# Optimization experiments

Measured on AMD Instinct MI355X. Metric: run time of the kernel, lower is better.

Reference implementation:

```python
import jax, jax.numpy as jnp
import numpy as np

C = 64            # x_channel (d_model)
D = 2 * C         # d_inner (expand=2)
N = C // 2        # d_state
K = 4             # scan directions
R = -(-C // 16)   # dt_rank = ceil(d_model/16)
Bsz, H, W = 2, 48, 48
EPS = 1e-5


def setup_inputs() -> dict:
    key = jax.random.key(0)
    ks = jax.random.split(key, 8)
    g = lambda k, shp, s: jax.random.normal(k, shp, dtype=jnp.float32) * s
    return {
        "fufea1": g(ks[0], (Bsz, C, H, W), 1.0),
        "ln_g": jnp.ones((C,), jnp.float32),
        "ln_b": jnp.zeros((C,), jnp.float32),
        "in_proj_w": g(ks[1], (2 * D, C), C ** -0.5),
        "conv_w": g(ks[2], (D, 1, 3, 3), 1.0 / 3.0),   # depthwise 3x3
        "conv_b": g(ks[3], (D,), 0.02),
        "x_proj_w": g(ks[4], (K, R + 2 * N, D), D ** -0.5),
        "dt_w": g(ks[5], (K, D, R), R ** -0.5),
        "dt_b": g(ks[6], (K, D), 0.1),
        "A_logs": jnp.log(jnp.tile(jnp.arange(1, N + 1, dtype=jnp.float32), (K, D, 1))),  # S4D-real init
        "Ds": jnp.ones((K, D), jnp.float32),
        "out_ln_g": jnp.ones((D,), jnp.float32),
        "out_ln_b": jnp.zeros((D,), jnp.float32),
        "out_proj_w": g(ks[7], (C, D), D ** -0.5),
    }


def _layernorm(x, g, b):
    mu = x.mean(-1, keepdims=True)
    var = ((x - mu) ** 2).mean(-1, keepdims=True)
    return (x - mu) * jax.lax.rsqrt(var + EPS) * g + b


def reference(fufea1, ln_g, ln_b, in_proj_w, conv_w, conv_b, x_proj_w,
              dt_w, dt_b, A_logs, Ds, out_ln_g, out_ln_b, out_proj_w):
    B, Cc, Hh, Ww = fufea1.shape
    L = Hh * Ww
    # pre-LN (over channels, channels-last)
    xn = _layernorm(fufea1.transpose(0, 2, 3, 1), ln_g, ln_b)          # (B,H,W,C)
    # SS2D: in_proj -> split x,z
    xz = xn @ in_proj_w.T                                               # (B,H,W,2D)
    x, z = jnp.split(xz, 2, axis=-1)
    x = x.transpose(0, 3, 1, 2)                                         # (B,D,H,W)
    x = jax.lax.conv_general_dilated(x, conv_w, (1, 1), "SAME",
                                     feature_group_count=D,
                                     dimension_numbers=("NCHW", "OIHW", "NCHW"))
    x = jax.nn.silu(x + conv_b[None, :, None, None])
    # 4-direction sequences: row-major, col-major, and their reverses
    x_hw = x.reshape(B, D, L)
    x_wh = x.transpose(0, 1, 3, 2).reshape(B, D, L)
    xs = jnp.stack([x_hw, x_wh], axis=1)                                # (B,2,D,L)
    xs = jnp.concatenate([xs, jnp.flip(xs, axis=-1)], axis=1)           # (B,K,D,L)
    # per-direction projections of dt, B, C
    x_dbl = jnp.einsum("bkdl,kcd->bkcl", xs, x_proj_w)
    dts, Bs, Cs = jnp.split(x_dbl, [R, R + N], axis=2)                  # (B,K,R,L),(B,K,N,L),(B,K,N,L)
    dts = jnp.einsum("bkrl,kdr->bkdl", dts, dt_w)
    delta = jax.nn.softplus(dts + dt_b[None, :, :, None])               # (B,K,D,L)
    A = -jnp.exp(A_logs)                                                # (K,D,N)
    # selective scan over L; carry h: (B,K,D,N)
    u_l = xs.transpose(3, 0, 1, 2)                                      # (L,B,K,D)
    dt_l = delta.transpose(3, 0, 1, 2)
    B_l = Bs.transpose(3, 0, 1, 2)                                      # (L,B,K,N)
    C_l = Cs.transpose(3, 0, 1, 2)

    def step(h, inp):
        u_t, d_t, b_t, c_t = inp
        dA = jnp.exp(d_t[..., None] * A)                                # (B,K,D,N)
        h = dA * h + (d_t * u_t)[..., None] * b_t[:, :, None, :]
        y = jnp.einsum("bkdn,bkn->bkd", h, c_t)
        return h, y

    h0 = jnp.zeros((B, K, D, N), xs.dtype)
    _, ys = jax.lax.scan(step, h0, (u_l, dt_l, B_l, C_l))               # ys: (L,B,K,D)
    out_y = ys.transpose(1, 2, 3, 0) + Ds[None, :, :, None] * xs        # (B,K,D,L)
    # merge the 4 directions back to row-major hw order
    inv_y = jnp.flip(out_y[:, 2:4], axis=-1)                            # (B,2,D,L)
    wh = lambda t: t.reshape(B, D, Ww, Hh).transpose(0, 1, 3, 2).reshape(B, D, L)
    y = out_y[:, 0] + inv_y[:, 0] + wh(out_y[:, 1]) + wh(inv_y[:, 1])   # (B,D,L)
    y = y.transpose(0, 2, 1).reshape(B, Hh, Ww, D)
    y = _layernorm(y, out_ln_g, out_ln_b) * jax.nn.silu(z)
    out = (y @ out_proj_w.T).transpose(0, 3, 1, 2) + fufea1             # residual add
    return out
```

## Files before the change

### kernel.cpp

```cpp
#include <hip/hip_runtime.h>

#define Cc 64
#define Dd 128
#define Nn 32
#define Kk 4
#define Rr 4
#define Bb 2
#define Hh 48
#define Ww 48
#define Ll 2304
#define EPSf 1e-5f
#define LCc 144

#if __has_builtin(__builtin_amdgcn_exp2f)
#define EXP2F __builtin_amdgcn_exp2f
#else
#define EXP2F exp2f
#endif

__device__ __forceinline__ float wsum64(float v) {
  v += __shfl_xor(v, 32);
  v += __shfl_xor(v, 16);
  v += __shfl_xor(v, 8);
  v += __shfl_xor(v, 4);
  v += __shfl_xor(v, 2);
  v += __shfl_xor(v, 1);
  return v;
}

__device__ __forceinline__ float hmax32(float v) {
  v = fmaxf(v, __shfl_xor(v, 1));
  v = fmaxf(v, __shfl_xor(v, 2));
  v = fmaxf(v, __shfl_xor(v, 4));
  v = fmaxf(v, __shfl_xor(v, 8));
  v = fmaxf(v, __shfl_xor(v, 16));
  return v;
}

__global__ __launch_bounds__(256) void k1_ln_inproj(
    const float* __restrict__ x, const float* __restrict__ g,
    const float* __restrict__ bta, const float* __restrict__ Wp,
    float* __restrict__ xin, float* __restrict__ zb)
{
  __shared__ float xS[16][65];
  __shared__ float xnS[16][64];
  __shared__ float xaS[128][17];
  const int tid = threadIdx.x;
  const int wv = tid >> 6, lane = tid & 63;
  const int pbase = blockIdx.x * 16;
  const int b = pbase / Ll;
  const int lbase = pbase % Ll;
  {
    const int c = tid >> 2, li0 = (tid & 3) * 4;
    const float4 v4 = *(const float4*)&x[(b * Cc + c) * Ll + lbase + li0];
    xS[li0 + 0][c] = v4.x;
    xS[li0 + 1][c] = v4.y;
    xS[li0 + 2][c] = v4.z;
    xS[li0 + 3][c] = v4.w;
  }
  __syncthreads();
  const float gv = g[lane], bv = bta[lane];
  for (int pi = 0; pi < 4; ++pi) {
    const int p = wv * 4 + pi;
    const float v = xS[p][lane];
    const float mu = wsum64(v) * (1.0f / 64.0f);
    const float dv = v - mu;
    const float var = wsum64(dv * dv) * (1.0f / 64.0f);
    const float rs = rsqrtf(var + EPSf);
    xnS[p][lane] = dv * rs * gv + bv;
  }
  __syncthreads();
  float acc[4][4];
  #pragma unroll
  for (int pi = 0; pi < 4; ++pi)
    #pragma unroll
    for (int m = 0; m < 4; ++m) acc[pi][m] = 0.f;
  const float4* W4 = (const float4*)Wp;
  #pragma unroll 4
  for (int c4 = 0; c4 < 16; ++c4) {
    float4 xn4[4];
    #pragma unroll
    for (int pi = 0; pi < 4; ++pi)
      xn4[pi] = ((const float4*)xnS[wv * 4 + pi])[c4];
    #pragma unroll
    for (int m = 0; m < 4; ++m) {
      const float4 w4 = W4[(lane + 64 * m) * 16 + c4];
      #pragma unroll
      for (int pi = 0; pi < 4; ++pi)
        acc[pi][m] += xn4[pi].x * w4.x + xn4[pi].y * w4.y +
                      xn4[pi].z * w4.z + xn4[pi].w * w4.w;
    }
  }
  #pragma unroll
  for (int pi = 0; pi < 4; ++pi) {
    const int l = lbase + wv * 4 + pi;
    zb[(b * Ll + l) * Dd + lane]      = acc[pi][2];
    zb[(b * Ll + l) * Dd + lane + 64] = acc[pi][3];
    xaS[lane][wv * 4 + pi]      = acc[pi][0];
    xaS[lane + 64][wv * 4 + pi] = acc[pi][1];
  }
  __syncthreads();
  const int d = tid >> 1, off = (tid & 1) * 8;
  float* dst = &xin[(b * Dd + d) * Ll + lbase + off];
  #pragma unroll
  for (int i = 0; i < 8; ++i) dst[i] = xaS[d][off + i];
}

__global__ __launch_bounds__(512) void k3_proj(
    const float* __restrict__ xin, const float* __restrict__ cw,
    const float* __restrict__ cb, const float* __restrict__ xpw,
    const float* __restrict__ dtw, const float* __restrict__ dtb,
    float* __restrict__ xc, float2* __restrict__ dd2,
    float* __restrict__ Bm, float* __restrict__ Cm)
{
  __shared__ float xinS[128][30];
  __shared__ float xvS[8][132];
  __shared__ float dtsS[8][16];
  const int t = threadIdx.x;
  const int pb = blockIdx.x * 8;
  const int b = pb / Ll;
  const int lb = pb % Ll;
  const int h0 = lb / Ww, w0 = lb % Ww;
  for (int i = t; i < 3840; i += 512) {
    const int d = i / 30, j = i % 30;
    const int r = j / 10, c = j % 10;
    const int hh = h0 + r - 1, ww = w0 + c - 1;
    float v = 0.f;
    if (hh >= 0 && hh < Hh && ww >= 0 && ww < Ww)
      v = xin[(b * Dd + d) * Ll + hh * Ww + ww];
    xinS[d][j] = v;
  }
  __syncthreads();
  for (int i = t; i < 1024; i += 512) {
    const int pi = i >> 7, d = i & 127;
    float acc = cb[d];
    #pragma unroll
    for (int r = 0; r < 3; ++r)
      #pragma unroll
      for (int c = 0; c < 3; ++c)
        acc += xinS[d][r * 10 + pi + c] * cw[d * 9 + r * 3 + c];
    const float sig = 1.0f / (1.0f + __expf(-acc));
    xvS[pi][d] = acc * sig;
  }
  __syncthreads();
  for (int i = t; i < 1024; i += 512) {
    const int d = i >> 3, pi = i & 7;
    xc[(b * Dd + d) * Ll + lb + pi] = xvS[pi][d];
  }
  if (t < 272) {
    const int k = t / 68, c = t % 68;
    const size_t bkL = (size_t)(b * Kk + k) * Ll;
    float acc[8];
    #pragma unroll
    for (int pi = 0; pi < 8; ++pi) acc[pi] = 0.f;
    const float4* w4p = (const float4*)(xpw + (k * 68 + c) * 128);
    for (int d4 = 0; d4 < 32; ++d4) {
      const float4 w4 = w4p[d4];
      #pragma unroll
      for (int pi = 0; pi < 8; ++pi) {
        const float4 x4 = ((const float4*)xvS[pi])[d4];
        acc[pi] += x4.x * w4.x + x4.y * w4.y + x4.z * w4.z + x4.w * w4.w;
      }
    }
    #pragma unroll
    for (int pi = 0; pi < 8; ++pi) {
      const int l0 = lb + pi;
      const int h = l0 / Ww, w = l0 % Ww;
      int lk;
      if      (k == 0) lk = l0;
      else if (k == 1) lk = w * Hh + h;
      else if (k == 2) lk = Ll - 1 - l0;
      else             lk = Ll - 1 - (w * Hh + h);
      if (c < Rr)            dtsS[pi][k * 4 + c] = acc[pi];
      else if (c < Rr + Nn)  Bm[(bkL + lk) * Nn + (c - Rr)] = acc[pi];
      else                   Cm[(bkL + lk) * Nn + (c - Rr - Nn)] = acc[pi];
    }
  }
  __syncthreads();
  {
    const int k = t >> 7, dd = t & 127;
    const float4 dw = *(const float4*)&dtw[(k * Dd + dd) * 4];
    const float biasv = dtb[k * Dd + dd];
    float2* drow = dd2 + ((size_t)((b * Kk + k) * Dd) + dd) * Ll;
    float2 buf[8];
    #pragma unroll
    for (int pi = 0; pi < 8; ++pi) {
      const float a = biasv
          + dtsS[pi][k * 4 + 0] * dw.x + dtsS[pi][k * 4 + 1] * dw.y
          + dtsS[pi][k * 4 + 2] * dw.z + dtsS[pi][k * 4 + 3] * dw.w;
      const float sp = (a > 20.f) ? a : log1pf(__expf(a));
      buf[pi] = make_float2(sp, sp * xvS[pi][dd]);
    }
    if (k == 0) {
      float4* f4 = (float4*)(drow + lb);
      #pragma unroll
      for (int j = 0; j < 4; ++j)
        f4[j] = make_float4(buf[2 * j].x, buf[2 * j].y, buf[2 * j + 1].x, buf[2 * j + 1].y);
    } else if (k == 2) {
      float4* f4 = (float4*)(drow + (Ll - 8 - lb));
      #pragma unroll
      for (int j = 0; j < 4; ++j)
        f4[j] = make_float4(buf[7 - 2 * j].x, buf[7 - 2 * j].y, buf[6 - 2 * j].x, buf[6 - 2 * j].y);
    } else {
      #pragma unroll
      for (int pi = 0; pi < 8; ++pi) {
        const int l0 = lb + pi;
        const int h = l0 / Ww, w = l0 % Ww;
        int lk = w * Hh + h;
        if (k == 3) lk = Ll - 1 - lk;
        drow[lk] = buf[pi];
      }
    }
  }
}

__global__ __launch_bounds__(512) void k4_scan(
    const float2* __restrict__ dd2, const float* __restrict__ Bm,
    const float* __restrict__ Cm, const float* __restrict__ Alogs,
    float* __restrict__ ys)
{
  __shared__ float hendS[16][32];
  __shared__ float carryS[16][32];
  __shared__ float sumDS[16];
  __shared__ float cmaxS[16];
  __shared__ float pS[16][8][36];
  const int tid = threadIdx.x;
  const int s = tid >> 5, n = tid & 31;
  const int blk = blockIdx.x;
  const int bk = blk & 7;
  const int d = blk >> 3;
  const int b = bk >> 2, k = bk & 3;
  const float An = -__expf(Alogs[(k * Dd + d) * Nn + n]);
  const float AnE = An * 1.44269504f;
  const size_t bkL = (size_t)(b * Kk + k) * Ll;
  const float2* dP = dd2 + ((size_t)((b * Kk + k) * Dd) + d) * Ll;
  const float* bP = Bm + bkL * Nn + n;
  const float* cP = Cm + bkL * Nn + n;
  const int lbeg = s * LCc;
  float* yP = ys + ((size_t)((b * Kk + k) * Dd) + d) * Ll + lbeg;
  const int rrow = n & 7, qtr = n >> 3;

  float h = 0.f, sumD = 0.f, cmx = 0.f;
  {
    const float4* q4 = (const float4*)(dP + lbeg);
    const float* bl = bP + (size_t)lbeg * Nn;
    const float* cl = cP + (size_t)lbeg * Nn;
    float4 qa = q4[0], qb = q4[1];
    float b0 = bl[0], b1 = bl[Nn], b2 = bl[2 * Nn], b3 = bl[3 * Nn];
    float c0 = cl[0], c1 = cl[Nn], c2 = cl[2 * Nn], c3 = cl[3 * Nn];
    for (int t8 = 0; t8 < LCc / 8; ++t8) {
      #pragma unroll
      for (int half = 0; half < 2; ++half) {
        q4 += 2; bl += 4 * Nn; cl += 4 * Nn;
        const float4 qa_n = q4[0], qb_n = q4[1];
        const float b0n = bl[0], b1n = bl[Nn], b2n = bl[2 * Nn], b3n = bl[3 * Nn];
        const float c0n = cl[0], c1n = cl[Nn], c2n = cl[2 * Nn], c3n = cl[3 * Nn];
        h = EXP2F(qa.x * AnE) * h + qa.y * b0; pS[s][half * 4 + 0][n] = h * c0;
        h = EXP2F(qa.z * AnE) * h + qa.w * b1; pS[s][half * 4 + 1][n] = h * c1;
        h = EXP2F(qb.x * AnE) * h + qb.y * b2; pS[s][half * 4 + 2][n] = h * c2;
        h = EXP2F(qb.z * AnE) * h + qb.w * b3; pS[s][half * 4 + 3][n] = h * c3;
        sumD += (qa.x + qa.z) + (qb.x + qb.z);
        cmx = fmaxf(cmx, fmaxf(fmaxf(fabsf(c0), fabsf(c1)),
                               fmaxf(fabsf(c2), fabsf(c3))));
        qa = qa_n; qb = qb_n; b0 = b0n; b1 = b1n; b2 = b2n; b3 = b3n;
        c0 = c0n; c1 = c1n; c2 = c2n; c3 = c3n;
      }
      const float4 a4 = *(const float4*)&pS[s][rrow][qtr * 8];
      const float4 d4v = *(const float4*)&pS[s][rrow][qtr * 8 + 4];
      float sum = ((a4.x + a4.y) + (a4.z + a4.w)) + ((d4v.x + d4v.y) + (d4v.z + d4v.w));
      sum += __shfl_xor(sum, 8);
      sum += __shfl_xor(sum, 16);
      if (n < 8) yP[t8 * 8 + n] = sum;
    }
  }
  hendS[s][n] = h;
  const float cmxAll = hmax32(cmx);
  if (n == 0) { sumDS[s] = sumD; cmaxS[s] = cmxAll; }
  __syncthreads();
  if (tid < 32) {
    float carry = 0.f;
    #pragma unroll
    for (int s2 = 0; s2 < 16; ++s2) {
      carryS[s2][tid] = carry;
      carry = EXP2F(AnE * sumDS[s2]) * carry + hendS[s2][tid];
    }
  }
  __syncthreads();
  const float carry = carryS[s][n];
  const float mc = hmax32(fabsf(carry));
  const float AmaxE = hmax32(AnE);
  const float Pstop = log2f(mc * cmaxS[s] * 3.2e6f) / (-AmaxE);
  {
    float hc = carry, P = 0.f;
    const float4* q4 = (const float4*)(dP + lbeg);
    const float* cl = cP + (size_t)lbeg * Nn;
    for (int t8 = 0; t8 < LCc / 8; ++t8) {
      if (!(P < Pstop)) break;
      #pragma unroll
      for (int half = 0; half < 2; ++half) {
        const float4 qa = q4[0], qb = q4[1];
        q4 += 2;
        hc *= EXP2F(qa.x * AnE); pS[s][half * 4 + 0][n] = hc * cl[0];
        hc *= EXP2F(qa.z * AnE); pS[s][half * 4 + 1][n] = hc * cl[Nn];
        hc *= EXP2F(qb.x * AnE); pS[s][half * 4 + 2][n] = hc * cl[2 * Nn];
        hc *= EXP2F(qb.z * AnE); pS[s][half * 4 + 3][n] = hc * cl[3 * Nn];
        P += (qa.x + qa.z) + (qb.x + qb.z);
        cl += 4 * Nn;
      }
      const float4 a4 = *(const float4*)&pS[s][rrow][qtr * 8];
      const float4 d4v = *(const float4*)&pS[s][rrow][qtr * 8 + 4];
      float sum = ((a4.x + a4.y) + (a4.z + a4.w)) + ((d4v.x + d4v.y) + (d4v.z + d4v.w));
      sum += __shfl_xor(sum, 8);
      sum += __shfl_xor(sum, 16);
      if (n < 8) yP[t8 * 8 + n] += sum;
    }
  }
}

__global__ __launch_bounds__(256) void k5_merge(
    const float* __restrict__ ys, const float* __restrict__ zb,
    const float* __restrict__ og, const float* __restrict__ ob,
    const float* __restrict__ Wo, const float* __restrict__ resid,
    const float* __restrict__ xc, const float* __restrict__ DsP,
    float* __restrict__ out)
{
  __shared__ float ysS[4][16][128];
  __shared__ float tS[16][128];
  __shared__ float oS[64][17];
  __shared__ float xcS[16][128];
  const int tid = threadIdx.x;
  const int wv = tid >> 6, lane = tid & 63;
  const int pbase = blockIdx.x * 16;
  const int b = pbase / Ll;
  const int lbase = pbase % Ll;
  const int hrow = lbase / Ww, w0 = lbase % Ww;
  {
    const int dch = tid & 127, seg = tid >> 7;
    {
      const float4 a4 = *(const float4*)&xc[(b * Dd + dch) * Ll + lbase + seg * 8];
      const float4 c4 = *(const float4*)&xc[(b * Dd + dch) * Ll + lbase + seg * 8 + 4];
      xcS[seg * 8 + 0][dch] = a4.x; xcS[seg * 8 + 1][dch] = a4.y;
      xcS[seg * 8 + 2][dch] = a4.z; xcS[seg * 8 + 3][dch] = a4.w;
      xcS[seg * 8 + 4][dch] = c4.x; xcS[seg * 8 + 5][dch] = c4.y;
      xcS[seg * 8 + 6][dch] = c4.z; xcS[seg * 8 + 7][dch] = c4.w;
    }
    {
      const size_t r0 = ((size_t)(b * Kk + 0) * Dd + dch) * Ll + lbase + seg * 8;
      const float4 a4 = *(const float4*)&ys[r0];
      const float4 c4 = *(const float4*)&ys[r0 + 4];
      ysS[0][seg * 8 + 0][dch] = a4.x; ysS[0][seg * 8 + 1][dch] = a4.y;
      ysS[0][seg * 8 + 2][dch] = a4.z; ysS[0][seg * 8 + 3][dch] = a4.w;
      ysS[0][seg * 8 + 4][dch] = c4.x; ysS[0][seg * 8 + 5][dch] = c4.y;
      ysS[0][seg * 8 + 6][dch] = c4.z; ysS[0][seg * 8 + 7][dch] = c4.w;
    }
    {
      const size_t r2 = ((size_t)(b * Kk + 2) * Dd + dch) * Ll + (Ll - 16 - lbase) + seg * 8;
      const float4 a4 = *(const float4*)&ys[r2];
      const float4 c4 = *(const float4*)&ys[r2 + 4];
      ysS[2][15 - seg * 8 - 0][dch] = a4.x; ysS[2][15 - seg * 8 - 1][dch] = a4.y;
      ysS[2][15 - seg * 8 - 2][dch] = a4.z; ysS[2][15 - seg * 8 - 3][dch] = a4.w;
      ysS[2][15 - seg * 8 - 4][dch] = c4.x; ysS[2][15 - seg * 8 - 5][dch] = c4.y;
      ysS[2][15 - seg * 8 - 6][dch] = c4.z; ysS[2][15 - seg * 8 - 7][dch] = c4.w;
    }
    {
      const size_t r1 = ((size_t)(b * Kk + 1) * Dd + dch) * Ll;
      const size_t r3 = ((size_t)(b * Kk + 3) * Dd + dch) * Ll;
      #pragma unroll
      for (int j = 0; j < 8; ++j) {
        const int p = seg * 8 + j;
        const int l1 = (w0 + p) * Hh + hrow;
        ysS[1][p][dch] = ys[r1 + l1];
        ysS[3][p][dch] = ys[r3 + (Ll - 1 - l1)];
      }
    }
  }
  float sDs[2];
  #pragma unroll
  for (int m = 0; m < 2; ++m) {
    const int dch = lane + 64 * m;
    sDs[m] = DsP[dch] + DsP[Dd + dch] + DsP[2 * Dd + dch] + DsP[3 * Dd + dch];
  }
  __syncthreads();
  for (int pi = 0; pi < 4; ++pi) {
    const int p = wv * 4 + pi;
    const int l0 = lbase + p;
    float tv[2];
    #pragma unroll
    for (int m = 0; m < 2; ++m) {
      const int dch = lane + 64 * m;
      tv[m] = ysS[0][p][dch] + ysS[1][p][dch] + ysS[2][p][dch] + ysS[3][p][dch]
            + sDs[m] * xcS[p][dch];
    }
    const float mu = wsum64(tv[0] + tv[1]) * (1.0f / 128.0f);
    const float q = wsum64((tv[0] - mu) * (tv[0] - mu) +
                           (tv[1] - mu) * (tv[1] - mu)) * (1.0f / 128.0f);
    const float rs = rsqrtf(q + EPSf);
    #pragma unroll
    for (int m = 0; m < 2; ++m) {
      const int dch = lane + 64 * m;
      const float zz = zb[(size_t)(b * Ll + l0) * Dd + dch];
      const float sig = 1.0f / (1.0f + __expf(-zz));
      tS[p][dch] = ((tv[m] - mu) * rs * og[dch] + ob[dch]) * (zz * sig);
    }
  }
  __syncthreads();
  float acc[4] = {0.f, 0.f, 0.f, 0.f};
  const float4* W4 = (const float4*)Wo;
  for (int d4 = 0; d4 < 32; ++d4) {
    const float4 w4 = W4[lane * 32 + d4];
    #pragma unroll
    for (int pi = 0; pi < 4; ++pi) {
      const float4 t4 = ((const float4*)tS[wv * 4 + pi])[d4];
      acc[pi] += t4.x * w4.x + t4.y * w4.y + t4.z * w4.z + t4.w * w4.w;
    }
  }
  #pragma unroll
  for (int pi = 0; pi < 4; ++pi) oS[lane][wv * 4 + pi] = acc[pi];
  __syncthreads();
  const int c = tid >> 2, off = (tid & 3) * 4;
  const size_t obase = (size_t)(b * Cc + c) * Ll + lbase + off;
  const float4 r4 = *(const float4*)(resid + obase);
  float4 o4;
  o4.x = oS[c][off + 0] + r4.x;
  o4.y = oS[c][off + 1] + r4.y;
  o4.z = oS[c][off + 2] + r4.z;
  o4.w = oS[c][off + 3] + r4.w;
  *(float4*)(out + obase) = o4;
}

extern "C" void kernel_launch(void* const* d_in, const int* in_sizes, int n_in,
                              void* d_out, int out_size, void* d_ws, size_t ws_size,
                              hipStream_t stream)
{
  (void)in_sizes; (void)n_in; (void)out_size; (void)ws_size;
  const float* fufea1     = (const float*)d_in[0];
  const float* ln_g       = (const float*)d_in[1];
  const float* ln_b       = (const float*)d_in[2];
  const float* in_proj_w  = (const float*)d_in[3];
  const float* conv_w     = (const float*)d_in[4];
  const float* conv_b     = (const float*)d_in[5];
  const float* x_proj_w   = (const float*)d_in[6];
  const float* dt_w       = (const float*)d_in[7];
  const float* dt_b       = (const float*)d_in[8];
  const float* A_logs     = (const float*)d_in[9];
  const float* Ds         = (const float*)d_in[10];
  const float* out_ln_g   = (const float*)d_in[11];
  const float* out_ln_b   = (const float*)d_in[12];
  const float* out_proj_w = (const float*)d_in[13];

  float* ws = (float*)d_ws;
  float2* dd2 = (float2*)ws;
  float* Bm   = ws + 4718592;
  float* Cm   = ws + 5308416;
  float* zb   = ws + 5898240;
  float* xc   = ws + 6488064;
  float* ysb  = ws + 7077888;
  float* xin  = ws + 7077888;

  k1_ln_inproj<<<288, 256, 0, stream>>>(fufea1, ln_g, ln_b, in_proj_w, xin, zb);
  k3_proj<<<576, 512, 0, stream>>>(xin, conv_w, conv_b, x_proj_w, dt_w, dt_b,
                                   xc, dd2, Bm, Cm);
  k4_scan<<<1024, 512, 0, stream>>>(dd2, Bm, Cm, A_logs, ysb);
  k5_merge<<<288, 256, 0, stream>>>(ysb, zb, out_ln_g, out_ln_b, out_proj_w, fufea1,
                                    xc, Ds, (float*)d_out);
}
```

Baseline: 202.6 us.

## Interleave B and C projections, tile merge kernel as 4x4 patches, overlap xc stores

B and C are stored interleaved as float2 pairs, so the scan loads one 8-byte value per step instead of two separate 4-byte loads from different arrays. The merge kernel now handles 4x4 spatial tiles instead of 16-pixel row segments, so the column-major directions can be read with float4 loads instead of strided scalar gathers. In the projection kernel, threads that sit idle during the x_proj GEMV now write xc in parallel with it. This costs more index arithmetic and a strided write pattern for the interleaved buffer.

```diff
diff --git a/kernel.cpp b/kernel.cpp
--- a/kernel.cpp
+++ b/kernel.cpp
@@ -111,7 +111,7 @@
     const float* __restrict__ cb, const float* __restrict__ xpw,
     const float* __restrict__ dtw, const float* __restrict__ dtb,
     float* __restrict__ xc, float2* __restrict__ dd2,
-    float* __restrict__ Bm, float* __restrict__ Cm)
+    float* __restrict__ BCm)
 {
   __shared__ float xinS[128][30];
   __shared__ float xvS[8][132];
@@ -143,10 +143,6 @@
     xvS[pi][d] = acc * sig;
   }
   __syncthreads();
-  for (int i = t; i < 1024; i += 512) {
-    const int d = i >> 3, pi = i & 7;
-    xc[(b * Dd + d) * Ll + lb + pi] = xvS[pi][d];
-  }
   if (t < 272) {
     const int k = t / 68, c = t % 68;
     const size_t bkL = (size_t)(b * Kk + k) * Ll;
@@ -171,9 +167,17 @@
       else if (k == 1) lk = w * Hh + h;
       else if (k == 2) lk = Ll - 1 - l0;
       else             lk = Ll - 1 - (w * Hh + h);
-      if (c < Rr)            dtsS[pi][k * 4 + c] = acc[pi];
-      else if (c < Rr + Nn)  Bm[(bkL + lk) * Nn + (c - Rr)] = acc[pi];
-      else                   Cm[(bkL + lk) * Nn + (c - Rr - Nn)] = acc[pi];
+      if (c < Rr)
+        dtsS[pi][k * 4 + c] = acc[pi];
+      else if (c < Rr + Nn)
+        BCm[((bkL + lk) * Nn + (c - Rr)) * 2]     = acc[pi];
+      else
+        BCm[((bkL + lk) * Nn + (c - Rr - Nn)) * 2 + 1] = acc[pi];
+    }
+  } else {
+    for (int i = t - 272; i < 1024; i += 240) {
+      const int d = i >> 3, pi = i & 7;
+      xc[(b * Dd + d) * Ll + lb + pi] = xvS[pi][d];
     }
   }
   __syncthreads();
@@ -215,9 +219,8 @@
 }
 
 __global__ __launch_bounds__(512) void k4_scan(
-    const float2* __restrict__ dd2, const float* __restrict__ Bm,
-    const float* __restrict__ Cm, const float* __restrict__ Alogs,
-    float* __restrict__ ys)
+    const float2* __restrict__ dd2, const float* __restrict__ BCm,
+    const float* __restrict__ Alogs, float* __restrict__ ys)
 {
   __shared__ float hendS[16][32];
   __shared__ float carryS[16][32];
@@ -234,8 +237,7 @@
   const float AnE = An * 1.44269504f;
   const size_t bkL = (size_t)(b * Kk + k) * Ll;
   const float2* dP = dd2 + ((size_t)((b * Kk + k) * Dd) + d) * Ll;
-  const float* bP = Bm + bkL * Nn + n;
-  const float* cP = Cm + bkL * Nn + n;
+  const float2* bcP = (const float2*)BCm + bkL * Nn + n;
   const int lbeg = s * LCc;
   float* yP = ys + ((size_t)((b * Kk + k) * Dd) + d) * Ll + lbeg;
   const int rrow = n & 7, qtr = n >> 3;
@@ -243,27 +245,23 @@
   float h = 0.f, sumD = 0.f, cmx = 0.f;
   {
     const float4* q4 = (const float4*)(dP + lbeg);
-    const float* bl = bP + (size_t)lbeg * Nn;
-    const float* cl = cP + (size_t)lbeg * Nn;
+    const float2* bcl = bcP + (size_t)lbeg * Nn;
     float4 qa = q4[0], qb = q4[1];
-    float b0 = bl[0], b1 = bl[Nn], b2 = bl[2 * Nn], b3 = bl[3 * Nn];
-    float c0 = cl[0], c1 = cl[Nn], c2 = cl[2 * Nn], c3 = cl[3 * Nn];
+    float2 bc0 = bcl[0], bc1 = bcl[Nn], bc2 = bcl[2 * Nn], bc3 = bcl[3 * Nn];
     for (int t8 = 0; t8 < LCc / 8; ++t8) {
       #pragma unroll
       for (int half = 0; half < 2; ++half) {
-        q4 += 2; bl += 4 * Nn; cl += 4 * Nn;
+        q4 += 2; bcl += 4 * Nn;
         const float4 qa_n = q4[0], qb_n = q4[1];
-        const float b0n = bl[0], b1n = bl[Nn], b2n = bl[2 * Nn], b3n = bl[3 * Nn];
-        const float c0n = cl[0], c1n = cl[Nn], c2n = cl[2 * Nn], c3n = cl[3 * Nn];
-        h = EXP2F(qa.x * AnE) * h + qa.y * b0; pS[s][half * 4 + 0][n] = h * c0;
-        h = EXP2F(qa.z * AnE) * h + qa.w * b1; pS[s][half * 4 + 1][n] = h * c1;
-        h = EXP2F(qb.x * AnE) * h + qb.y * b2; pS[s][half * 4 + 2][n] = h * c2;
-        h = EXP2F(qb.z * AnE) * h + qb.w * b3; pS[s][half * 4 + 3][n] = h * c3;
+        const float2 bc0n = bcl[0], bc1n = bcl[Nn], bc2n = bcl[2 * Nn], bc3n = bcl[3 * Nn];
+        h = EXP2F(qa.x * AnE) * h + qa.y * bc0.x; pS[s][half * 4 + 0][n] = h * bc0.y;
+        h = EXP2F(qa.z * AnE) * h + qa.w * bc1.x; pS[s][half * 4 + 1][n] = h * bc1.y;
+        h = EXP2F(qb.x * AnE) * h + qb.y * bc2.x; pS[s][half * 4 + 2][n] = h * bc2.y;
+        h = EXP2F(qb.z * AnE) * h + qb.w * bc3.x; pS[s][half * 4 + 3][n] = h * bc3.y;
         sumD += (qa.x + qa.z) + (qb.x + qb.z);
-        cmx = fmaxf(cmx, fmaxf(fmaxf(fabsf(c0), fabsf(c1)),
-                               fmaxf(fabsf(c2), fabsf(c3))));
-        qa = qa_n; qb = qb_n; b0 = b0n; b1 = b1n; b2 = b2n; b3 = b3n;
-        c0 = c0n; c1 = c1n; c2 = c2n; c3 = c3n;
+        cmx = fmaxf(cmx, fmaxf(fmaxf(fabsf(bc0.y), fabsf(bc1.y)),
+                               fmaxf(fabsf(bc2.y), fabsf(bc3.y))));
+        qa = qa_n; qb = qb_n; bc0 = bc0n; bc1 = bc1n; bc2 = bc2n; bc3 = bc3n;
       }
       const float4 a4 = *(const float4*)&pS[s][rrow][qtr * 8];
       const float4 d4v = *(const float4*)&pS[s][rrow][qtr * 8 + 4];
@@ -293,17 +291,17 @@
   {
     float hc = carry, P = 0.f;
     const float4* q4 = (const float4*)(dP + lbeg);
-    const float* cl = cP + (size_t)lbeg * Nn;
+    const float2* cl = bcP + (size_t)lbeg * Nn;
     for (int t8 = 0; t8 < LCc / 8; ++t8) {
       if (!(P < Pstop)) break;
       #pragma unroll
       for (int half = 0; half < 2; ++half) {
         const float4 qa = q4[0], qb = q4[1];
         q4 += 2;
-        hc *= EXP2F(qa.x * AnE); pS[s][half * 4 + 0][n] = hc * cl[0];
-        hc *= EXP2F(qa.z * AnE); pS[s][half * 4 + 1][n] = hc * cl[Nn];
-        hc *= EXP2F(qb.x * AnE); pS[s][half * 4 + 2][n] = hc * cl[2 * Nn];
-        hc *= EXP2F(qb.z * AnE); pS[s][half * 4 + 3][n] = hc * cl[3 * Nn];
+        hc *= EXP2F(qa.x * AnE); pS[s][half * 4 + 0][n] = hc * cl[0].y;
+        hc *= EXP2F(qa.z * AnE); pS[s][half * 4 + 1][n] = hc * cl[Nn].y;
+        hc *= EXP2F(qb.x * AnE); pS[s][half * 4 + 2][n] = hc * cl[2 * Nn].y;
+        hc *= EXP2F(qb.z * AnE); pS[s][half * 4 + 3][n] = hc * cl[3 * Nn].y;
         P += (qa.x + qa.z) + (qb.x + qb.z);
         cl += 4 * Nn;
       }
@@ -330,48 +328,40 @@
   __shared__ float xcS[16][128];
   const int tid = threadIdx.x;
   const int wv = tid >> 6, lane = tid & 63;
-  const int pbase = blockIdx.x * 16;
-  const int b = pbase / Ll;
-  const int lbase = pbase % Ll;
-  const int hrow = lbase / Ww, w0 = lbase % Ww;
+  const int tb = blockIdx.x;
+  const int b = tb / 144;
+  const int ti = tb % 144;
+  const int tr = ti / 12, tc = ti % 12;
+  const int h0 = tr * 4, w0 = tc * 4;
   {
-    const int dch = tid & 127, seg = tid >> 7;
-    {
-      const float4 a4 = *(const float4*)&xc[(b * Dd + dch) * Ll + lbase + seg * 8];
-      const float4 c4 = *(const float4*)&xc[(b * Dd + dch) * Ll + lbase + seg * 8 + 4];
-      xcS[seg * 8 + 0][dch] = a4.x; xcS[seg * 8 + 1][dch] = a4.y;
-      xcS[seg * 8 + 2][dch] = a4.z; xcS[seg * 8 + 3][dch] = a4.w;
-      xcS[seg * 8 + 4][dch] = c4.x; xcS[seg * 8 + 5][dch] = c4.y;
-      xcS[seg * 8 + 6][dch] = c4.z; xcS[seg * 8 + 7][dch] = c4.w;
-    }
-    {
-      const size_t r0 = ((size_t)(b * Kk + 0) * Dd + dch) * Ll + lbase + seg * 8;
-      const float4 a4 = *(const float4*)&ys[r0];
-      const float4 c4 = *(const float4*)&ys[r0 + 4];
-      ysS[0][seg * 8 + 0][dch] = a4.x; ysS[0][seg * 8 + 1][dch] = a4.y;
-      ysS[0][seg * 8 + 2][dch] = a4.z; ysS[0][seg * 8 + 3][dch] = a4.w;
-      ysS[0][seg * 8 + 4][dch] = c4.x; ysS[0][seg * 8 + 5][dch] = c4.y;
-      ysS[0][seg * 8 + 6][dch] = c4.z; ysS[0][seg * 8 + 7][dch] = c4.w;
-    }
-    {
-      const size_t r2 = ((size_t)(b * Kk + 2) * Dd + dch) * Ll + (Ll - 16 - lbase) + seg * 8;
-      const float4 a4 = *(const float4*)&ys[r2];
-      const float4 c4 = *(const float4*)&ys[r2 + 4];
-      ysS[2][15 - seg * 8 - 0][dch] = a4.x; ysS[2][15 - seg * 8 - 1][dch] = a4.y;
-      ysS[2][15 - seg * 8 - 2][dch] = a4.z; ysS[2][15 - seg * 8 - 3][dch] = a4.w;
-      ysS[2][15 - seg * 8 - 4][dch] = c4.x; ysS[2][15 - seg * 8 - 5][dch] = c4.y;
-      ysS[2][15 - seg * 8 - 6][dch] = c4.z; ysS[2][15 - seg * 8 - 7][dch] = c4.w;
-    }
-    {
-      const size_t r1 = ((size_t)(b * Kk + 1) * Dd + dch) * Ll;
-      const size_t r3 = ((size_t)(b * Kk + 3) * Dd + dch) * Ll;
-      #pragma unroll
-      for (int j = 0; j < 8; ++j) {
-        const int p = seg * 8 + j;
-        const int l1 = (w0 + p) * Hh + hrow;
-        ysS[1][p][dch] = ys[r1 + l1];
-        ysS[3][p][dch] = ys[r3 + (Ll - 1 - l1)];
-      }
+    const int dch = tid & 127, half = tid >> 7;
+    #pragma unroll
+    for (int ii = 0; ii < 2; ++ii) {
+      const int i = half * 2 + ii;
+      const int l0 = (h0 + i) * Ww + w0;
+      float4 v;
+      v = *(const float4*)&xc[(b * Dd + dch) * Ll + l0];
+      xcS[i * 4 + 0][dch] = v.x; xcS[i * 4 + 1][dch] = v.y;
+      xcS[i * 4 + 2][dch] = v.z; xcS[i * 4 + 3][dch] = v.w;
+      v = *(const float4*)&ys[((size_t)(b * Kk + 0) * Dd + dch) * Ll + l0];
+      ysS[0][i * 4 + 0][dch] = v.x; ysS[0][i * 4 + 1][dch] = v.y;
+      ysS[0][i * 4 + 2][dch] = v.z; ysS[0][i * 4 + 3][dch] = v.w;
+      const int r2 = Ll - 4 - (h0 + i) * Ww - w0;
+      v = *(const float4*)&ys[((size_t)(b * Kk + 2) * Dd + dch) * Ll + r2];
+      ysS[2][i * 4 + 3][dch] = v.x; ysS[2][i * 4 + 2][dch] = v.y;
+      ysS[2][i * 4 + 1][dch] = v.z; ysS[2][i * 4 + 0][dch] = v.w;
+    }
+    #pragma unroll
+    for (int jj = 0; jj < 2; ++jj) {
+      const int j = half * 2 + jj;
+      const int l1 = (w0 + j) * Hh + h0;
+      float4 v = *(const float4*)&ys[((size_t)(b * Kk + 1) * Dd + dch) * Ll + l1];
+      ysS[1][0 * 4 + j][dch] = v.x; ysS[1][1 * 4 + j][dch] = v.y;
+      ysS[1][2 * 4 + j][dch] = v.z; ysS[1][3 * 4 + j][dch] = v.w;
+      const int r3 = Ll - 4 - (w0 + j) * Hh - h0;
+      v = *(const float4*)&ys[((size_t)(b * Kk + 3) * Dd + dch) * Ll + r3];
+      ysS[3][3 * 4 + j][dch] = v.x; ysS[3][2 * 4 + j][dch] = v.y;
+      ysS[3][1 * 4 + j][dch] = v.z; ysS[3][0 * 4 + j][dch] = v.w;
     }
   }
   float sDs[2];
@@ -383,7 +373,7 @@
   __syncthreads();
   for (int pi = 0; pi < 4; ++pi) {
     const int p = wv * 4 + pi;
-    const int l0 = lbase + p;
+    const int l0 = (h0 + (p >> 2)) * Ww + w0 + (p & 3);
     float tv[2];
     #pragma unroll
     for (int m = 0; m < 2; ++m) {
@@ -417,14 +407,14 @@
   #pragma unroll
   for (int pi = 0; pi < 4; ++pi) oS[lane][wv * 4 + pi] = acc[pi];
   __syncthreads();
-  const int c = tid >> 2, off = (tid & 3) * 4;
-  const size_t obase = (size_t)(b * Cc + c) * Ll + lbase + off;
+  const int c = tid >> 2, q = tid & 3;
+  const size_t obase = (size_t)(b * Cc + c) * Ll + (size_t)(h0 + q) * Ww + w0;
   const float4 r4 = *(const float4*)(resid + obase);
   float4 o4;
-  o4.x = oS[c][off + 0] + r4.x;
-  o4.y = oS[c][off + 1] + r4.y;
-  o4.z = oS[c][off + 2] + r4.z;
-  o4.w = oS[c][off + 3] + r4.w;
+  o4.x = oS[c][q * 4 + 0] + r4.x;
+  o4.y = oS[c][q * 4 + 1] + r4.y;
+  o4.z = oS[c][q * 4 + 2] + r4.z;
+  o4.w = oS[c][q * 4 + 3] + r4.w;
   *(float4*)(out + obase) = o4;
 }
 
@@ -450,8 +440,7 @@
 
   float* ws = (float*)d_ws;
   float2* dd2 = (float2*)ws;
-  float* Bm   = ws + 4718592;
-  float* Cm   = ws + 5308416;
+  float* BCm  = ws + 4718592;
   float* zb   = ws + 5898240;
   float* xc   = ws + 6488064;
   float* ysb  = ws + 7077888;
@@ -459,8 +448,8 @@
 
   k1_ln_inproj<<<288, 256, 0, stream>>>(fufea1, ln_g, ln_b, in_proj_w, xin, zb);
   k3_proj<<<576, 512, 0, stream>>>(xin, conv_w, conv_b, x_proj_w, dt_w, dt_b,
-                                   xc, dd2, Bm, Cm);
-  k4_scan<<<1024, 512, 0, stream>>>(dd2, Bm, Cm, A_logs, ysb);
+                                   xc, dd2, BCm);
+  k4_scan<<<1024, 512, 0, stream>>>(dd2, BCm, A_logs, ysb);
   k5_merge<<<288, 256, 0, stream>>>(ysb, zb, out_ln_g, out_ln_b, out_proj_w, fufea1,
                                     xc, Ds, (float*)d_out);
 }
```

Measured after the change: 224.2 us. +10.6%, slower.
